# Performance work log

Measured on AMD Instinct MI355X. Metric: run time of the kernel, lower is better.

Reference implementation:

```python
import jax, jax.numpy as jnp
import numpy as np

EPS = 1e-5

def _bn(t, gamma, beta):
    # training-mode BatchNorm2d: stats over (B,H,W), biased variance
    mean = jnp.mean(t, axis=(0, 2, 3), keepdims=True)
    var = jnp.var(t, axis=(0, 2, 3), keepdims=True)
    tn = (t - mean) * jax.lax.rsqrt(var + EPS)
    return tn * gamma[None, :, None, None] + beta[None, :, None, None]

def setup_inputs() -> dict:
    key = jax.random.key(0)
    ks = jax.random.split(key, 8)
    B, C, H, W = 16, 256, 64, 64
    u, k, v = 4, 16, 256
    s = 1.0 / np.sqrt(C)
    x = jax.random.normal(ks[0], (B, C, H, W), dtype=jnp.float32)
    Wq = jax.random.normal(ks[1], (k, C), dtype=jnp.float32) * s
    bq = jax.random.normal(ks[2], (k,), dtype=jnp.float32) * 0.01
    Wk = jax.random.normal(ks[3], (u * k, C), dtype=jnp.float32) * s
    bk = jax.random.normal(ks[4], (u * k,), dtype=jnp.float32) * 0.01
    Wv = jax.random.normal(ks[5], (u * v, C), dtype=jnp.float32) * s
    bv = jax.random.normal(ks[6], (u * v,), dtype=jnp.float32) * 0.01
    gamma_q = jnp.ones((k,), dtype=jnp.float32)
    beta_q = jnp.zeros((k,), dtype=jnp.float32)
    gamma_v = jnp.ones((u * v,), dtype=jnp.float32)
    beta_v = jnp.zeros((u * v,), dtype=jnp.float32)
    return {"x": x, "Wq": Wq, "bq": bq, "Wk": Wk, "bk": bk, "Wv": Wv, "bv": bv,
            "gamma_q": gamma_q, "beta_q": beta_q, "gamma_v": gamma_v, "beta_v": beta_v}

def reference(x, Wq, bq, Wk, bk, Wv, bv, gamma_q, beta_q, gamma_v, beta_v):
    B, C, H, W = x.shape
    k = Wq.shape[0]
    u = 4
    v = Wv.shape[0] // u
    # 1x1 convs as channel contractions
    Q = jnp.einsum('oc,bchw->bohw', Wq, x) + bq[None, :, None, None]   # [B,k,H,W]
    K = jnp.einsum('oc,bchw->bohw', Wk, x) + bk[None, :, None, None]   # [B,u*k,H,W]
    V = jnp.einsum('oc,bchw->bohw', Wv, x) + bv[None, :, None, None]   # [B,u*v,H,W]
    Q = _bn(Q, gamma_q, beta_q)
    V = _bn(V, gamma_v, beta_v)
    m = H * W
    Q = Q.reshape(B, k, m)          # [B,k,m]
    K = K.reshape(B, u, k, m)       # [B,u,k,m]
    V = V.reshape(B, u, v, m)       # [B,u,v,m]
    K = jax.nn.softmax(K, axis=3)
    context = jnp.einsum('bukm,buvm->bkv', K, V)   # [B,k,v]
    y = jnp.einsum('bkn,bkv->bvn', Q, context)     # [B,v,m]
    return y.reshape(B, v, H, W)
```

## Files before the change

kernel.cpp:

```cpp
#include <hip/hip_runtime.h>
#include <hip/hip_bf16.h>

typedef short s16x8 __attribute__((ext_vector_type(8)));
typedef short s16x4 __attribute__((ext_vector_type(4)));
typedef float f32x4 __attribute__((ext_vector_type(4)));
typedef unsigned u32;
typedef u32 u32x2 __attribute__((ext_vector_type(2)));

#define DI __device__ __forceinline__

constexpr int BB = 16;
constexpr int CC = 256;
constexpr int MM = 4096;
constexpr int KD = 16;
constexpr int UK = 64;
constexpr float EPSV = 1e-5f;

DI unsigned short f2bf(float f) {
  union { float f; unsigned u; } v; v.f = f;
  unsigned r = v.u + 0x7FFFu + ((v.u >> 16) & 1u);
  return (unsigned short)(r >> 16);
}
DI float bflo(u32 v) { union { u32 u; float f; } w; w.u = v << 16; return w.f; }
DI float bfhi(u32 v) { union { u32 u; float f; } w; w.u = v & 0xFFFF0000u; return w.f; }

__global__ __launch_bounds__(256) void k_cvt(const float* __restrict__ x,
    unsigned short* __restrict__ xbf, float* __restrict__ xsump) {
  int bid = blockIdx.x;
  size_t base = (size_t)bid * MM;
  int t = threadIdx.x;
  float s = 0.f;
#pragma unroll
  for (int i = 0; i < 4; ++i) {
    size_t idx = base + (size_t)(i * 256 + t) * 4;
    float4 v = *(const float4*)(x + idx);
    s16x4 c;
    c[0] = (short)f2bf(v.x); c[1] = (short)f2bf(v.y);
    c[2] = (short)f2bf(v.z); c[3] = (short)f2bf(v.w);
    *(s16x4*)&xbf[idx] = c;
    s += v.x + v.y + v.z + v.w;
  }
#pragma unroll
  for (int o = 32; o; o >>= 1) s += __shfl_down(s, o);
  __shared__ float red[4];
  if ((t & 63) == 0) red[t >> 6] = s;
  __syncthreads();
  if (t == 0) xsump[bid] = red[0] + red[1] + red[2] + red[3];
}

__global__ __launch_bounds__(512) void k_gxx(const unsigned short* __restrict__ xbf,
                                             u32* __restrict__ part) {
  int b = blockIdx.x >> 4, mc = blockIdx.x & 15;
  int m0 = mc * 256;
  __shared__ short lds[2][256 * 72];
  int t = threadIdx.x, w = t >> 6, l = t & 63;
  int wr = w >> 2, wc = w & 3;
  int lrow = l & 15, lk8 = (l >> 4) * 8;
  int srow = t >> 3, sseg = (t & 7) * 8;

  const unsigned short* gsrc = xbf + ((size_t)(b * CC + srow)) * MM + m0 + sseg;

  s16x8 rg[4];
#pragma unroll
  for (int i = 0; i < 4; ++i)
    rg[i] = *(const s16x8*)(gsrc + (size_t)i * 64 * MM);
#pragma unroll
  for (int i = 0; i < 4; ++i)
    *(s16x8*)&lds[0][(srow + i * 64) * 72 + sseg] = rg[i];

  f32x4 acc[8][4];
#pragma unroll
  for (int i = 0; i < 8; ++i)
#pragma unroll
    for (int j = 0; j < 4; ++j) acc[i][j] = (f32x4)0.f;

#pragma unroll
  for (int ks = 0; ks < 4; ++ks) {
    __syncthreads();
    if (ks < 3) {
#pragma unroll
      for (int i = 0; i < 4; ++i)
        rg[i] = *(const s16x8*)(gsrc + (size_t)i * 64 * MM + (ks + 1) * 64);
    }
    int buf = ks & 1;
#pragma unroll
    for (int half = 0; half < 2; ++half) {
      s16x8 af[8], bf[4];
#pragma unroll
      for (int i = 0; i < 8; ++i)
        af[i] = *(const s16x8*)&lds[buf][(wr * 128 + i * 16 + lrow) * 72 + half * 32 + lk8];
#pragma unroll
      for (int j = 0; j < 4; ++j)
        bf[j] = *(const s16x8*)&lds[buf][(wc * 64 + j * 16 + lrow) * 72 + half * 32 + lk8];
#pragma unroll
      for (int i = 0; i < 8; ++i)
#pragma unroll
        for (int j = 0; j < 4; ++j)
          acc[i][j] = __builtin_amdgcn_mfma_f32_16x16x32_bf16(af[i], bf[j], acc[i][j], 0, 0, 0);
    }
    if (ks < 3) {
#pragma unroll
      for (int i = 0; i < 4; ++i)
        *(s16x8*)&lds[buf ^ 1][(srow + i * 64) * 72 + sseg] = rg[i];
    }
  }

  size_t pb = (size_t)blockIdx.x * 32768;
#pragma unroll
  for (int i = 0; i < 8; ++i)
#pragma unroll
    for (int j = 0; j < 4; ++j) {
      int tau = (w * 8 + i) * 4 + j;
      u32x2 pk;
      pk[0] = (u32)f2bf(acc[i][j][0]) | ((u32)f2bf(acc[i][j][1]) << 16);
      pk[1] = (u32)f2bf(acc[i][j][2]) | ((u32)f2bf(acc[i][j][3]) << 16);
      *(u32x2*)&part[pb + tau * 128 + l * 2] = pk;
    }
}

__global__ __launch_bounds__(256) void k_gred(const u32* __restrict__ part,
                                              float* __restrict__ G) {
  int q = blockIdx.x * 256 + threadIdx.x;
  float s0 = 0.f, s1 = 0.f;
#pragma unroll 8
  for (int p = 0; p < 256; ++p) {
    u32 v = part[(size_t)p * 32768 + q];
    s0 += bflo(v);
    s1 += bfhi(v);
  }
  int r2 = q & 1, l = (q >> 1) & 63, tau = q >> 7;
  int j = tau & 3, i = (tau >> 2) & 7, w = tau >> 5;
  int wr = w >> 2, wc = w & 3;
  int row = wr * 128 + i * 16 + (l >> 4) * 4 + r2 * 2;
  int col = wc * 64 + j * 16 + (l & 15);
  G[row * 256 + col] = s0;
  G[(row + 1) * 256 + col] = s1;
}

__global__ __launch_bounds__(256) void k_proj(const unsigned short* __restrict__ xbf,
    const float* __restrict__ Wq, const float* __restrict__ bq,
    const float* __restrict__ Wk, const float* __restrict__ bk,
    float* __restrict__ Kb, float* __restrict__ Qb) {
  int b = blockIdx.x >> 5, mc = blockIdx.x & 31;
  int gm0 = mc * 128;
  __shared__ short wlds[80 * 264];
  __shared__ u32 xt[128 * 17];
  int t = threadIdx.x;
  int w = t >> 6, l = t & 63;
  int lrow = l & 15, lk = l >> 4;

#pragma unroll 4
  for (int o = 0; o < 80; ++o) {
    float v = (o < 64) ? Wk[o * CC + t] : Wq[(o - 64) * CC + t];
    wlds[o * 264 + t] = (short)f2bf(v);
  }

  f32x4 acc[5][2];
#pragma unroll
  for (int i = 0; i < 5; ++i) { acc[i][0] = (f32x4)0.f; acc[i][1] = (f32x4)0.f; }

  int c2 = t >> 4;
  int mq = t & 15;

  for (int ks = 0; ks < 8; ++ks) {
    int c0 = ks * 32;
    __syncthreads();
#pragma unroll
    for (int mb = 0; mb < 128; mb += 64) {
      int m = mb + mq * 4;
      const unsigned short* p0 = xbf + ((size_t)(b * CC + c0 + 2 * c2)) * MM + gm0 + m;
      s16x4 v0 = *(const s16x4*)p0;
      s16x4 v1 = *(const s16x4*)(p0 + MM);
      xt[(m + 0) * 17 + c2] = (u32)(unsigned short)v0[0] | ((u32)(unsigned short)v1[0] << 16);
      xt[(m + 1) * 17 + c2] = (u32)(unsigned short)v0[1] | ((u32)(unsigned short)v1[1] << 16);
      xt[(m + 2) * 17 + c2] = (u32)(unsigned short)v0[2] | ((u32)(unsigned short)v1[2] << 16);
      xt[(m + 3) * 17 + c2] = (u32)(unsigned short)v0[3] | ((u32)(unsigned short)v1[3] << 16);
    }
    __syncthreads();
    union { s16x8 v; u32 wd[4]; } bfr[2];
#pragma unroll
    for (int j = 0; j < 2; ++j) {
      int ml = w * 32 + j * 16 + lrow;
#pragma unroll
      for (int i = 0; i < 4; ++i) bfr[j].wd[i] = xt[ml * 17 + lk * 4 + i];
    }
#pragma unroll
    for (int ot = 0; ot < 5; ++ot) {
      s16x8 af = *(const s16x8*)&wlds[(ot * 16 + lrow) * 264 + c0 + lk * 8];
      acc[ot][0] = __builtin_amdgcn_mfma_f32_16x16x32_bf16(af, bfr[0].v, acc[ot][0], 0, 0, 0);
      acc[ot][1] = __builtin_amdgcn_mfma_f32_16x16x32_bf16(af, bfr[1].v, acc[ot][1], 0, 0, 0);
    }
  }

#pragma unroll
  for (int ot = 0; ot < 5; ++ot)
#pragma unroll
    for (int j = 0; j < 2; ++j)
#pragma unroll
      for (int r = 0; r < 4; ++r) {
        int o = ot * 16 + lk * 4 + r;
        int m = gm0 + w * 32 + j * 16 + lrow;
        float val = acc[ot][j][r];
        if (o < 64) Kb[((size_t)(b * UK + o)) * MM + m] = val + bk[o];
        else        Qb[((size_t)(b * KD + o - 64)) * MM + m] = val + bq[o - 64];
      }
}

__global__ __launch_bounds__(256) void k_sstats(const float* __restrict__ Kb,
    float* __restrict__ rmax, float* __restrict__ rsum) {
  int r = blockIdx.x;
  int t = threadIdx.x;
  const float4* p = (const float4*)(Kb + (size_t)r * MM);
  float4 v[4];
  float mx = -3.4e38f;
#pragma unroll
  for (int i = 0; i < 4; ++i) {
    v[i] = p[i * 256 + t];
    mx = fmaxf(mx, fmaxf(fmaxf(v[i].x, v[i].y), fmaxf(v[i].z, v[i].w)));
  }
#pragma unroll
  for (int o = 32; o; o >>= 1) mx = fmaxf(mx, __shfl_xor(mx, o));
  __shared__ float red[4];
  int w = t >> 6;
  if ((t & 63) == 0) red[w] = mx;
  __syncthreads();
  mx = fmaxf(fmaxf(red[0], red[1]), fmaxf(red[2], red[3]));
  float s = 0.f;
#pragma unroll
  for (int i = 0; i < 4; ++i)
    s += __expf(v[i].x - mx) + __expf(v[i].y - mx) +
         __expf(v[i].z - mx) + __expf(v[i].w - mx);
#pragma unroll
  for (int o = 32; o; o >>= 1) s += __shfl_xor(s, o);
  __syncthreads();
  if ((t & 63) == 0) red[w] = s;
  __syncthreads();
  if (t == 0) {
    rmax[r] = mx;
    rsum[r] = red[0] + red[1] + red[2] + red[3];
  }
}

__global__ __launch_bounds__(256) void k_fin(const float* __restrict__ G,
    const float* __restrict__ xsump,
    const float* __restrict__ Wv, const float* __restrict__ bv,
    const float* __restrict__ gv, const float* __restrict__ btv,
    const float* __restrict__ Wq, const float* __restrict__ bq,
    const float* __restrict__ gq, const float* __restrict__ btq,
    float* __restrict__ AV, float* __restrict__ BVa,
    float* __restrict__ AQ, float* __restrict__ BQa) {
  int t = threadIdx.x, w = t >> 6, l = t & 63;
  int o0 = blockIdx.x * 4;
  __shared__ float lw[4][256];
#pragma unroll
  for (int oo = 0; oo < 4; ++oo) {
    int o = o0 + oo;
    lw[oo][t] = (o < 1024) ? Wv[(size_t)o * CC + t] : Wq[(size_t)(o - 1024) * CC + t];
  }
  __syncthreads();

  float4 w4[4];
#pragma unroll
  for (int oo = 0; oo < 4; ++oo) w4[oo] = *(const float4*)&lw[oo][4 * l];

  float qf[4] = {0.f, 0.f, 0.f, 0.f};
#pragma unroll 4
  for (int i = 0; i < 64; ++i) {
    int r = i * 4 + w;
    float4 g4 = *(const float4*)(G + (size_t)r * CC + 4 * l);
#pragma unroll
    for (int oo = 0; oo < 4; ++oo) {
      float d = g4.x * w4[oo].x + g4.y * w4[oo].y + g4.z * w4[oo].z + g4.w * w4[oo].w;
      qf[oo] = fmaf(lw[oo][r], d, qf[oo]);
    }
  }

  float xs = 0.f;
#pragma unroll
  for (int bb = 0; bb < 16; ++bb) xs += xsump[bb * 256 + t];
  float sx[4];
#pragma unroll
  for (int oo = 0; oo < 4; ++oo) sx[oo] = lw[oo][t] * xs;

#pragma unroll
  for (int oo = 0; oo < 4; ++oo)
#pragma unroll
    for (int od = 32; od; od >>= 1) {
      qf[oo] += __shfl_xor(qf[oo], od);
      sx[oo] += __shfl_xor(sx[oo], od);
    }
  __shared__ float rq[4][4], rs[4][4];
  if (l == 0)
#pragma unroll
    for (int oo = 0; oo < 4; ++oo) { rq[w][oo] = qf[oo]; rs[w][oo] = sx[oo]; }
  __syncthreads();
  if (t < 4) {
    int oo = t, o = o0 + oo;
    float q = rq[0][oo] + rq[1][oo] + rq[2][oo] + rq[3][oo];
    float s = rs[0][oo] + rs[1][oo] + rs[2][oo] + rs[3][oo];
    float bias, gamma, beta; float *pa, *pb;
    if (o < 1024) { bias = bv[o]; gamma = gv[o]; beta = btv[o]; pa = AV + o; pb = BVa + o; }
    else { int oi = o - 1024; bias = bq[oi]; gamma = gq[oi]; beta = btq[oi]; pa = AQ + oi; pb = BQa + oi; }
    const float invN = 1.f / 65536.f;
    float mean = s * invN + bias;
    float e2 = q * invN + 2.f * bias * s * invN + bias * bias;
    float var = e2 - mean * mean;
    float a = gamma * rsqrtf(var + EPSV);
    *pa = a;
    *pb = beta - mean * a;
  }
}

__global__ __launch_bounds__(256) void k_xp(const unsigned short* __restrict__ xbf,
    const float* __restrict__ Kb, const float* __restrict__ rmax,
    float* __restrict__ xpp) {
  int b = blockIdx.x >> 4, kc = blockIdx.x & 15;
  int kbase = kc * 256;
  __shared__ short la[64][40];
  __shared__ short lb[256][40];
  int t = threadIdx.x, w = t >> 6, l = t & 63;
  int lrow = l & 15, lk = (l >> 4) * 8;

  f32x4 acc[4][4];
#pragma unroll
  for (int i = 0; i < 4; ++i)
#pragma unroll
    for (int j = 0; j < 4; ++j) acc[i][j] = (f32x4)0.f;

  for (int ks = 0; ks < 8; ++ks) {
    int k0 = kbase + ks * 32;
    __syncthreads();
    {
      int r = t >> 2, sg = (t & 3) * 8;
      const float4* src = (const float4*)(Kb + ((size_t)(b * UK + r)) * MM + k0 + sg);
      float rm = rmax[b * UK + r];
      s16x8 wv;
#pragma unroll
      for (int i = 0; i < 2; ++i) {
        float4 v = src[i];
        wv[i * 4 + 0] = (short)f2bf(__expf(v.x - rm));
        wv[i * 4 + 1] = (short)f2bf(__expf(v.y - rm));
        wv[i * 4 + 2] = (short)f2bf(__expf(v.z - rm));
        wv[i * 4 + 3] = (short)f2bf(__expf(v.w - rm));
      }
      *(s16x8*)&la[r][sg] = wv;
    }
#pragma unroll
    for (int i = 0; i < 4; ++i) {
      int r = i * 64 + (t >> 2), sg = (t & 3) * 8;
      s16x8 v = *(const s16x8*)&xbf[((size_t)(b * CC + r)) * MM + k0 + sg];
      *(s16x8*)&lb[r][sg] = v;
    }
    __syncthreads();
    s16x8 af[4], bfr[4];
#pragma unroll
    for (int i = 0; i < 4; ++i) af[i] = *(const s16x8*)&la[i * 16 + lrow][lk];
#pragma unroll
    for (int j = 0; j < 4; ++j) bfr[j] = *(const s16x8*)&lb[w * 64 + j * 16 + lrow][lk];
#pragma unroll
    for (int i = 0; i < 4; ++i)
#pragma unroll
      for (int j = 0; j < 4; ++j)
        acc[i][j] = __builtin_amdgcn_mfma_f32_16x16x32_bf16(af[i], bfr[j], acc[i][j], 0, 0, 0);
  }
  float* dst = xpp + (size_t)blockIdx.x * UK * CC;
#pragma unroll
  for (int i = 0; i < 4; ++i)
#pragma unroll
    for (int j = 0; j < 4; ++j)
#pragma unroll
      for (int r = 0; r < 4; ++r) {
        int row = i * 16 + (l >> 4) * 4 + r;
        int col = w * 64 + j * 16 + lrow;
        dst[row * 256 + col] = acc[i][j][r];
      }
}

__global__ __launch_bounds__(256) void k_xpn(const float* __restrict__ xpp,
    const float* __restrict__ rsum, unsigned short* __restrict__ xpn) {
  int b = blockIdx.x >> 4, kk = blockIdx.x & 15;
  int t = threadIdx.x;
  unsigned short* dst = xpn + ((size_t)(b * 16 + kk)) * 1024;
#pragma unroll
  for (int u = 0; u < 4; ++u) {
    int row = u * 16 + kk;
    float s = 0.f;
#pragma unroll
    for (int kc = 0; kc < 16; ++kc)
      s += xpp[((size_t)(b * 16 + kc) * UK + row) * CC + t];
    s /= rsum[b * UK + row];
    dst[u * 256 + t] = f2bf(s);
  }
}

__global__ __launch_bounds__(256) void k_wvs(const float* __restrict__ Wv,
    const float* __restrict__ AV, unsigned short* __restrict__ wvs) {
  int ch = blockIdx.x;
  int t = threadIdx.x;
  float a = AV[ch];
  wvs[(size_t)ch * CC + t] = f2bf(a * Wv[(size_t)ch * CC + t]);
}

__global__ __launch_bounds__(64) void k_ctx2(const unsigned short* __restrict__ xpn,
    const unsigned short* __restrict__ wvs,
    const float* __restrict__ AV, const float* __restrict__ bv,
    const float* __restrict__ BVa, float* __restrict__ CTX) {
  int mt = blockIdx.x >> 3, nt = blockIdx.x & 7;
  int m0 = mt * 32, n0 = nt * 32;
  int l = threadIdx.x;
  int lrow = l & 15, lk8 = (l >> 4) * 8;

  f32x4 acc[2][2];
#pragma unroll
  for (int i = 0; i < 2; ++i)
#pragma unroll
    for (int j = 0; j < 2; ++j) acc[i][j] = (f32x4)0.f;

#pragma unroll 4
  for (int k0 = 0; k0 < 1024; k0 += 32) {
    int u = k0 >> 8, c0 = k0 & 255;
    s16x8 a0 = *(const s16x8*)&xpn[(size_t)(m0 + lrow) * 1024 + k0 + lk8];
    s16x8 a1 = *(const s16x8*)&xpn[(size_t)(m0 + 16 + lrow) * 1024 + k0 + lk8];
    s16x8 b0 = *(const s16x8*)&wvs[(size_t)(u * 256 + n0 + lrow) * CC + c0 + lk8];
    s16x8 b1 = *(const s16x8*)&wvs[(size_t)(u * 256 + n0 + 16 + lrow) * CC + c0 + lk8];
    acc[0][0] = __builtin_amdgcn_mfma_f32_16x16x32_bf16(a0, b0, acc[0][0], 0, 0, 0);
    acc[0][1] = __builtin_amdgcn_mfma_f32_16x16x32_bf16(a0, b1, acc[0][1], 0, 0, 0);
    acc[1][0] = __builtin_amdgcn_mfma_f32_16x16x32_bf16(a1, b0, acc[1][0], 0, 0, 0);
    acc[1][1] = __builtin_amdgcn_mfma_f32_16x16x32_bf16(a1, b1, acc[1][1], 0, 0, 0);
  }

  float cst[2];
#pragma unroll
  for (int j = 0; j < 2; ++j) {
    int vv = n0 + j * 16 + lrow;
    float s = 0.f;
#pragma unroll
    for (int u = 0; u < 4; ++u) {
      int ch = u * 256 + vv;
      s += AV[ch] * bv[ch] + BVa[ch];
    }
    cst[j] = s;
  }

#pragma unroll
  for (int i = 0; i < 2; ++i)
#pragma unroll
    for (int j = 0; j < 2; ++j)
#pragma unroll
      for (int r = 0; r < 4; ++r) {
        int row = m0 + i * 16 + (l >> 4) * 4 + r;
        int col = n0 + j * 16 + lrow;
        CTX[(size_t)row * 256 + col] = acc[i][j][r] + cst[j];
      }
}

__global__ __launch_bounds__(256) void k_y(const float* __restrict__ Qb,
    const float* __restrict__ CTX,
    const float* __restrict__ AQ, const float* __restrict__ BQa,
    float* __restrict__ y) {
  int b = blockIdx.x >> 4, nc = blockIdx.x & 15;
  int m = nc * 256 + threadIdx.x;
  float qn[16];
#pragma unroll
  for (int kk = 0; kk < 16; ++kk)
    qn[kk] = AQ[kk] * Qb[((size_t)b * KD + kk) * MM + m] + BQa[kk];
  const float* cb = CTX + (size_t)b * KD * 256;
  float* yo = y + (size_t)b * 256 * MM + m;
#pragma unroll 4
  for (int vv = 0; vv < 256; ++vv) {
    float acc = 0.f;
#pragma unroll
    for (int kk = 0; kk < 16; ++kk)
      acc = fmaf(qn[kk], cb[kk * 256 + vv], acc);
    yo[(size_t)vv * MM] = acc;
  }
}

extern "C" void kernel_launch(void* const* d_in, const int* in_sizes, int n_in,
                              void* d_out, int out_size, void* d_ws, size_t ws_size,
                              hipStream_t stream) {
  const float* x   = (const float*)d_in[0];
  const float* Wq  = (const float*)d_in[1];
  const float* bq  = (const float*)d_in[2];
  const float* Wk  = (const float*)d_in[3];
  const float* bk  = (const float*)d_in[4];
  const float* Wv  = (const float*)d_in[5];
  const float* bv  = (const float*)d_in[6];
  const float* gq  = (const float*)d_in[7];
  const float* btq = (const float*)d_in[8];
  const float* gv  = (const float*)d_in[9];
  const float* btv = (const float*)d_in[10];
  float* out = (float*)d_out;
  float* ws  = (float*)d_ws;

  float* G     = ws;
  float* XSUMP = ws + 65536;
  float* RMAX  = ws + 69632;
  float* RSUM  = ws + 70656;
  float* AV    = ws + 71680;
  float* BVa   = ws + 72704;
  float* AQ    = ws + 73728;
  float* BQa   = ws + 73744;
  float* CTX   = ws + 73984;
  float* XPP   = ws + 139520;
  float* KB    = ws + 4333824;
  float* QB    = ws + 8528128;
  u32*  PART   = (u32*)(ws + 139520);
  unsigned short* XBF = (unsigned short*)(ws + 9576704);
  unsigned short* XPN = (unsigned short*)(ws + 17965312);
  unsigned short* WVS = (unsigned short*)(ws + 18096384);

  k_cvt   <<<4096, 256, 0, stream>>>(x, XBF, XSUMP);
  k_gxx   <<<256,  512, 0, stream>>>(XBF, PART);
  k_gred  <<<128,  256, 0, stream>>>(PART, G);
  k_proj  <<<512,  256, 0, stream>>>(XBF, Wq, bq, Wk, bk, KB, QB);
  k_sstats<<<1024, 256, 0, stream>>>(KB, RMAX, RSUM);
  k_fin   <<<260,  256, 0, stream>>>(G, XSUMP, Wv, bv, gv, btv, Wq, bq, gq, btq,
                                     AV, BVa, AQ, BQa);
  k_xp    <<<256,  256, 0, stream>>>(XBF, KB, RMAX, XPP);
  k_xpn   <<<256,  256, 0, stream>>>(XPP, RSUM, XPN);
  k_wvs   <<<1024, 256, 0, stream>>>(Wv, AV, WVS);
  k_ctx2  <<<64,   64,  0, stream>>>(XPN, WVS, AV, bv, BVa, CTX);
  k_y     <<<256,  256, 0, stream>>>(QB, CTX, AQ, BQa, out);
}
```

Baseline: 145.5 us.

## Fuse bf16 conversion into Gram kernel, fold softmax stats into projection, store K/Q as bf16

The fp32-to-bf16 conversion of x and the per-channel sums move into the Gram-matrix kernel, so x is read once instead of being converted in a separate pass. The projection kernel now writes K and Q as bf16 and computes per-tile online softmax max/sum, which a small merge kernel combines. This replaces the full-row statistics pass over fp32 K. The xpn and wvs kernels are merged into one launch. Fewer launches and less global traffic are the aim, at the cost of storing K and Q at bf16 precision and a larger xsump reduction in k_fin.

```diff
diff --git a/kernel.cpp b/kernel.cpp
--- a/kernel.cpp
+++ b/kernel.cpp
@@ -21,35 +21,23 @@
   unsigned r = v.u + 0x7FFFu + ((v.u >> 16) & 1u);
   return (unsigned short)(r >> 16);
 }
+DI float bfu(unsigned short u) { union { u32 u; float f; } w; w.u = (u32)u << 16; return w.f; }
 DI float bflo(u32 v) { union { u32 u; float f; } w; w.u = v << 16; return w.f; }
 DI float bfhi(u32 v) { union { u32 u; float f; } w; w.u = v & 0xFFFF0000u; return w.f; }
 
-__global__ __launch_bounds__(256) void k_cvt(const float* __restrict__ x,
-    unsigned short* __restrict__ xbf, float* __restrict__ xsump) {
-  int bid = blockIdx.x;
-  size_t base = (size_t)bid * MM;
-  int t = threadIdx.x;
-  float s = 0.f;
-#pragma unroll
-  for (int i = 0; i < 4; ++i) {
-    size_t idx = base + (size_t)(i * 256 + t) * 4;
-    float4 v = *(const float4*)(x + idx);
-    s16x4 c;
-    c[0] = (short)f2bf(v.x); c[1] = (short)f2bf(v.y);
-    c[2] = (short)f2bf(v.z); c[3] = (short)f2bf(v.w);
-    *(s16x4*)&xbf[idx] = c;
-    s += v.x + v.y + v.z + v.w;
-  }
-#pragma unroll
-  for (int o = 32; o; o >>= 1) s += __shfl_down(s, o);
-  __shared__ float red[4];
-  if ((t & 63) == 0) red[t >> 6] = s;
-  __syncthreads();
-  if (t == 0) xsump[bid] = red[0] + red[1] + red[2] + red[3];
-}
-
-__global__ __launch_bounds__(512) void k_gxx(const unsigned short* __restrict__ xbf,
-                                             u32* __restrict__ part) {
+DI s16x8 cvt8(const float4 a, const float4 b, float& s) {
+  s16x8 c;
+  c[0] = (short)f2bf(a.x); c[1] = (short)f2bf(a.y);
+  c[2] = (short)f2bf(a.z); c[3] = (short)f2bf(a.w);
+  c[4] = (short)f2bf(b.x); c[5] = (short)f2bf(b.y);
+  c[6] = (short)f2bf(b.z); c[7] = (short)f2bf(b.w);
+  s += a.x + a.y + a.z + a.w + b.x + b.y + b.z + b.w;
+  return c;
+}
+
+__global__ __launch_bounds__(512) void k_gcv(const float* __restrict__ x,
+    unsigned short* __restrict__ xbf, float* __restrict__ xsump,
+    u32* __restrict__ part) {
   int b = blockIdx.x >> 4, mc = blockIdx.x & 15;
   int m0 = mc * 256;
   __shared__ short lds[2][256 * 72];
@@ -58,15 +46,24 @@
   int lrow = l & 15, lk8 = (l >> 4) * 8;
   int srow = t >> 3, sseg = (t & 7) * 8;
 
-  const unsigned short* gsrc = xbf + ((size_t)(b * CC + srow)) * MM + m0 + sseg;
-
-  s16x8 rg[4];
-#pragma unroll
-  for (int i = 0; i < 4; ++i)
-    rg[i] = *(const s16x8*)(gsrc + (size_t)i * 64 * MM);
-#pragma unroll
-  for (int i = 0; i < 4; ++i)
-    *(s16x8*)&lds[0][(srow + i * 64) * 72 + sseg] = rg[i];
+  const float* gsrc = x + ((size_t)(b * CC + srow)) * MM + m0 + sseg;
+  unsigned short* xdst = xbf + ((size_t)(b * CC + srow)) * MM + m0 + sseg;
+
+  float rs4[4] = {0.f, 0.f, 0.f, 0.f};
+  float4 rf[4][2];
+
+#pragma unroll
+  for (int i = 0; i < 4; ++i) {
+    const float* p = gsrc + (size_t)i * 64 * MM;
+    rf[i][0] = *(const float4*)p;
+    rf[i][1] = *(const float4*)(p + 4);
+  }
+#pragma unroll
+  for (int i = 0; i < 4; ++i) {
+    s16x8 c = cvt8(rf[i][0], rf[i][1], rs4[i]);
+    *(s16x8*)&lds[0][(srow + i * 64) * 72 + sseg] = c;
+    *(s16x8*)&xdst[(size_t)i * 64 * MM] = c;
+  }
 
   f32x4 acc[8][4];
 #pragma unroll
@@ -79,8 +76,11 @@
     __syncthreads();
     if (ks < 3) {
 #pragma unroll
-      for (int i = 0; i < 4; ++i)
-        rg[i] = *(const s16x8*)(gsrc + (size_t)i * 64 * MM + (ks + 1) * 64);
+      for (int i = 0; i < 4; ++i) {
+        const float* p = gsrc + (size_t)i * 64 * MM + (ks + 1) * 64;
+        rf[i][0] = *(const float4*)p;
+        rf[i][1] = *(const float4*)(p + 4);
+      }
     }
     int buf = ks & 1;
 #pragma unroll
@@ -100,9 +100,19 @@
     }
     if (ks < 3) {
 #pragma unroll
-      for (int i = 0; i < 4; ++i)
-        *(s16x8*)&lds[buf ^ 1][(srow + i * 64) * 72 + sseg] = rg[i];
-    }
+      for (int i = 0; i < 4; ++i) {
+        s16x8 c = cvt8(rf[i][0], rf[i][1], rs4[i]);
+        *(s16x8*)&lds[buf ^ 1][(srow + i * 64) * 72 + sseg] = c;
+        *(s16x8*)&xdst[(size_t)i * 64 * MM + (ks + 1) * 64] = c;
+      }
+    }
+  }
+
+#pragma unroll
+  for (int i = 0; i < 4; ++i) {
+    float s = rs4[i];
+    s += __shfl_xor(s, 1); s += __shfl_xor(s, 2); s += __shfl_xor(s, 4);
+    if ((t & 7) == 0) xsump[blockIdx.x * 256 + srow + i * 64] = s;
   }
 
   size_t pb = (size_t)blockIdx.x * 32768;
@@ -140,11 +150,13 @@
 __global__ __launch_bounds__(256) void k_proj(const unsigned short* __restrict__ xbf,
     const float* __restrict__ Wq, const float* __restrict__ bq,
     const float* __restrict__ Wk, const float* __restrict__ bk,
-    float* __restrict__ Kb, float* __restrict__ Qb) {
+    unsigned short* __restrict__ Kbf, unsigned short* __restrict__ Qbf,
+    float* __restrict__ pstat) {
   int b = blockIdx.x >> 5, mc = blockIdx.x & 31;
   int gm0 = mc * 128;
   __shared__ short wlds[80 * 264];
   __shared__ u32 xt[128 * 17];
+  __shared__ float smax[4][64], ssum[4][64];
   int t = threadIdx.x;
   int w = t >> 6, l = t & 63;
   int lrow = l & 15, lk = l >> 4;
@@ -192,53 +204,66 @@
     }
   }
 
-#pragma unroll
-  for (int ot = 0; ot < 5; ++ot)
-#pragma unroll
-    for (int j = 0; j < 2; ++j)
-#pragma unroll
-      for (int r = 0; r < 4; ++r) {
-        int o = ot * 16 + lk * 4 + r;
-        int m = gm0 + w * 32 + j * 16 + lrow;
-        float val = acc[ot][j][r];
-        if (o < 64) Kb[((size_t)(b * UK + o)) * MM + m] = val + bk[o];
-        else        Qb[((size_t)(b * KD + o - 64)) * MM + m] = val + bq[o - 64];
-      }
-}
-
-__global__ __launch_bounds__(256) void k_sstats(const float* __restrict__ Kb,
+  int mcol = gm0 + w * 32 + lrow;
+#pragma unroll
+  for (int ot = 0; ot < 4; ++ot)
+#pragma unroll
+    for (int r = 0; r < 4; ++r) {
+      int o = ot * 16 + lk * 4 + r;
+      float bias = bk[o];
+      unsigned short u0 = f2bf(acc[ot][0][r] + bias);
+      unsigned short u1 = f2bf(acc[ot][1][r] + bias);
+      size_t rowoff = ((size_t)(b * UK + o)) * MM;
+      Kbf[rowoff + mcol] = u0;
+      Kbf[rowoff + mcol + 16] = u1;
+      float rv0 = bfu(u0), rv1 = bfu(u1);
+      float mx = fmaxf(rv0, rv1);
+      mx = fmaxf(mx, __shfl_xor(mx, 1));
+      mx = fmaxf(mx, __shfl_xor(mx, 2));
+      mx = fmaxf(mx, __shfl_xor(mx, 4));
+      mx = fmaxf(mx, __shfl_xor(mx, 8));
+      float se = __expf(rv0 - mx) + __expf(rv1 - mx);
+      se += __shfl_xor(se, 1);
+      se += __shfl_xor(se, 2);
+      se += __shfl_xor(se, 4);
+      se += __shfl_xor(se, 8);
+      if (lrow == 0) { smax[w][o] = mx; ssum[w][o] = se; }
+    }
+#pragma unroll
+  for (int r = 0; r < 4; ++r) {
+    int oq = lk * 4 + r;
+    float bias = bq[oq];
+    size_t rowoff = ((size_t)(b * KD + oq)) * MM;
+    Qbf[rowoff + mcol] = f2bf(acc[4][0][r] + bias);
+    Qbf[rowoff + mcol + 16] = f2bf(acc[4][1][r] + bias);
+  }
+  __syncthreads();
+  if (t < 64) {
+    float m0_ = smax[0][t], m1_ = smax[1][t], m2_ = smax[2][t], m3_ = smax[3][t];
+    float mm = fmaxf(fmaxf(m0_, m1_), fmaxf(m2_, m3_));
+    float ss = ssum[0][t] * __expf(m0_ - mm) + ssum[1][t] * __expf(m1_ - mm) +
+               ssum[2][t] * __expf(m2_ - mm) + ssum[3][t] * __expf(m3_ - mm);
+    size_t po = ((size_t)blockIdx.x * 64 + t) * 2;
+    pstat[po] = mm;
+    pstat[po + 1] = ss;
+  }
+}
+
+__global__ __launch_bounds__(64) void k_pmerge(const float* __restrict__ pstat,
     float* __restrict__ rmax, float* __restrict__ rsum) {
-  int r = blockIdx.x;
-  int t = threadIdx.x;
-  const float4* p = (const float4*)(Kb + (size_t)r * MM);
-  float4 v[4];
-  float mx = -3.4e38f;
-#pragma unroll
-  for (int i = 0; i < 4; ++i) {
-    v[i] = p[i * 256 + t];
-    mx = fmaxf(mx, fmaxf(fmaxf(v[i].x, v[i].y), fmaxf(v[i].z, v[i].w)));
-  }
-#pragma unroll
-  for (int o = 32; o; o >>= 1) mx = fmaxf(mx, __shfl_xor(mx, o));
-  __shared__ float red[4];
-  int w = t >> 6;
-  if ((t & 63) == 0) red[w] = mx;
-  __syncthreads();
-  mx = fmaxf(fmaxf(red[0], red[1]), fmaxf(red[2], red[3]));
-  float s = 0.f;
-#pragma unroll
-  for (int i = 0; i < 4; ++i)
-    s += __expf(v[i].x - mx) + __expf(v[i].y - mx) +
-         __expf(v[i].z - mx) + __expf(v[i].w - mx);
-#pragma unroll
-  for (int o = 32; o; o >>= 1) s += __shfl_xor(s, o);
-  __syncthreads();
-  if ((t & 63) == 0) red[w] = s;
-  __syncthreads();
-  if (t == 0) {
-    rmax[r] = mx;
-    rsum[r] = red[0] + red[1] + red[2] + red[3];
-  }
+  int b = blockIdx.x, o = threadIdx.x;
+  float mm = -3.4e38f;
+#pragma unroll 8
+  for (int mc = 0; mc < 32; ++mc)
+    mm = fmaxf(mm, pstat[((size_t)((b * 32 + mc) * 64 + o)) * 2]);
+  float ss = 0.f;
+#pragma unroll 8
+  for (int mc = 0; mc < 32; ++mc) {
+    size_t po = ((size_t)((b * 32 + mc) * 64 + o)) * 2;
+    ss += pstat[po + 1] * __expf(pstat[po] - mm);
+  }
+  rmax[b * 64 + o] = mm;
+  rsum[b * 64 + o] = ss;
 }
 
 __global__ __launch_bounds__(256) void k_fin(const float* __restrict__ G,
@@ -276,8 +301,8 @@
   }
 
   float xs = 0.f;
-#pragma unroll
-  for (int bb = 0; bb < 16; ++bb) xs += xsump[bb * 256 + t];
+#pragma unroll 8
+  for (int p = 0; p < 256; ++p) xs += xsump[p * 256 + t];
   float sx[4];
 #pragma unroll
   for (int oo = 0; oo < 4; ++oo) sx[oo] = lw[oo][t] * xs;
@@ -312,7 +337,7 @@
 }
 
 __global__ __launch_bounds__(256) void k_xp(const unsigned short* __restrict__ xbf,
-    const float* __restrict__ Kb, const float* __restrict__ rmax,
+    const unsigned short* __restrict__ Kbf, const float* __restrict__ rmax,
     float* __restrict__ xpp) {
   int b = blockIdx.x >> 4, kc = blockIdx.x & 15;
   int kbase = kc * 256;
@@ -332,17 +357,12 @@
     __syncthreads();
     {
       int r = t >> 2, sg = (t & 3) * 8;
-      const float4* src = (const float4*)(Kb + ((size_t)(b * UK + r)) * MM + k0 + sg);
+      s16x8 kv = *(const s16x8*)&Kbf[((size_t)(b * UK + r)) * MM + k0 + sg];
       float rm = rmax[b * UK + r];
       s16x8 wv;
 #pragma unroll
-      for (int i = 0; i < 2; ++i) {
-        float4 v = src[i];
-        wv[i * 4 + 0] = (short)f2bf(__expf(v.x - rm));
-        wv[i * 4 + 1] = (short)f2bf(__expf(v.y - rm));
-        wv[i * 4 + 2] = (short)f2bf(__expf(v.z - rm));
-        wv[i * 4 + 3] = (short)f2bf(__expf(v.w - rm));
-      }
+      for (int i = 0; i < 8; ++i)
+        wv[i] = (short)f2bf(__expf(bfu((unsigned short)kv[i]) - rm));
       *(s16x8*)&la[r][sg] = wv;
     }
 #pragma unroll
@@ -376,29 +396,29 @@
       }
 }
 
-__global__ __launch_bounds__(256) void k_xpn(const float* __restrict__ xpp,
-    const float* __restrict__ rsum, unsigned short* __restrict__ xpn) {
-  int b = blockIdx.x >> 4, kk = blockIdx.x & 15;
+__global__ __launch_bounds__(256) void k_prep(const float* __restrict__ xpp,
+    const float* __restrict__ rsum, const float* __restrict__ Wv,
+    const float* __restrict__ AV, unsigned short* __restrict__ xpn,
+    unsigned short* __restrict__ wvs) {
   int t = threadIdx.x;
-  unsigned short* dst = xpn + ((size_t)(b * 16 + kk)) * 1024;
-#pragma unroll
-  for (int u = 0; u < 4; ++u) {
-    int row = u * 16 + kk;
-    float s = 0.f;
-#pragma unroll
-    for (int kc = 0; kc < 16; ++kc)
-      s += xpp[((size_t)(b * 16 + kc) * UK + row) * CC + t];
-    s /= rsum[b * UK + row];
-    dst[u * 256 + t] = f2bf(s);
-  }
-}
-
-__global__ __launch_bounds__(256) void k_wvs(const float* __restrict__ Wv,
-    const float* __restrict__ AV, unsigned short* __restrict__ wvs) {
-  int ch = blockIdx.x;
-  int t = threadIdx.x;
-  float a = AV[ch];
-  wvs[(size_t)ch * CC + t] = f2bf(a * Wv[(size_t)ch * CC + t]);
+  if (blockIdx.x < 256) {
+    int b = blockIdx.x >> 4, kk = blockIdx.x & 15;
+    unsigned short* dst = xpn + ((size_t)(b * 16 + kk)) * 1024;
+#pragma unroll
+    for (int u = 0; u < 4; ++u) {
+      int row = u * 16 + kk;
+      float s = 0.f;
+#pragma unroll
+      for (int kc = 0; kc < 16; ++kc)
+        s += xpp[((size_t)(b * 16 + kc) * UK + row) * CC + t];
+      s /= rsum[b * UK + row];
+      dst[u * 256 + t] = f2bf(s);
+    }
+  } else {
+    int ch = blockIdx.x - 256;
+    float a = AV[ch];
+    wvs[(size_t)ch * CC + t] = f2bf(a * Wv[(size_t)ch * CC + t]);
+  }
 }
 
 __global__ __launch_bounds__(64) void k_ctx2(const unsigned short* __restrict__ xpn,
@@ -454,7 +474,7 @@
       }
 }
 
-__global__ __launch_bounds__(256) void k_y(const float* __restrict__ Qb,
+__global__ __launch_bounds__(256) void k_y(const unsigned short* __restrict__ Qbf,
     const float* __restrict__ CTX,
     const float* __restrict__ AQ, const float* __restrict__ BQa,
     float* __restrict__ y) {
@@ -463,7 +483,7 @@
   float qn[16];
 #pragma unroll
   for (int kk = 0; kk < 16; ++kk)
-    qn[kk] = AQ[kk] * Qb[((size_t)b * KD + kk) * MM + m] + BQa[kk];
+    qn[kk] = AQ[kk] * bfu(Qbf[((size_t)b * KD + kk) * MM + m]) + BQa[kk];
   const float* cb = CTX + (size_t)b * KD * 256;
   float* yo = y + (size_t)b * 256 * MM + m;
 #pragma unroll 4
@@ -495,31 +515,30 @@
 
   float* G     = ws;
   float* XSUMP = ws + 65536;
-  float* RMAX  = ws + 69632;
-  float* RSUM  = ws + 70656;
-  float* AV    = ws + 71680;
-  float* BVa   = ws + 72704;
-  float* AQ    = ws + 73728;
-  float* BQa   = ws + 73744;
-  float* CTX   = ws + 73984;
-  float* XPP   = ws + 139520;
-  float* KB    = ws + 4333824;
-  float* QB    = ws + 8528128;
-  u32*  PART   = (u32*)(ws + 139520);
-  unsigned short* XBF = (unsigned short*)(ws + 9576704);
-  unsigned short* XPN = (unsigned short*)(ws + 17965312);
-  unsigned short* WVS = (unsigned short*)(ws + 18096384);
-
-  k_cvt   <<<4096, 256, 0, stream>>>(x, XBF, XSUMP);
-  k_gxx   <<<256,  512, 0, stream>>>(XBF, PART);
+  float* PSTAT = ws + 131072;
+  float* RMAX  = ws + 196608;
+  float* RSUM  = ws + 197632;
+  float* AV    = ws + 198656;
+  float* BVa   = ws + 199680;
+  float* AQ    = ws + 200704;
+  float* BQa   = ws + 200720;
+  float* CTX   = ws + 200960;
+  u32*  PART   = (u32*)(ws + 266496);
+  float* XPP   = ws + 266496;
+  unsigned short* KBf = (unsigned short*)(ws + 4460800);
+  unsigned short* QBf = (unsigned short*)(ws + 6557952);
+  unsigned short* XBF = (unsigned short*)(ws + 8655104);
+  unsigned short* XPN = (unsigned short*)(ws + 17043712);
+  unsigned short* WVS = (unsigned short*)(ws + 17174784);
+
+  k_gcv   <<<256,  512, 0, stream>>>(x, XBF, XSUMP, PART);
   k_gred  <<<128,  256, 0, stream>>>(PART, G);
-  k_proj  <<<512,  256, 0, stream>>>(XBF, Wq, bq, Wk, bk, KB, QB);
-  k_sstats<<<1024, 256, 0, stream>>>(KB, RMAX, RSUM);
+  k_proj  <<<512,  256, 0, stream>>>(XBF, Wq, bq, Wk, bk, KBf, QBf, PSTAT);
+  k_pmerge<<<16,   64,  0, stream>>>(PSTAT, RMAX, RSUM);
   k_fin   <<<260,  256, 0, stream>>>(G, XSUMP, Wv, bv, gv, btv, Wq, bq, gq, btq,
                                      AV, BVa, AQ, BQa);
-  k_xp    <<<256,  256, 0, stream>>>(XBF, KB, RMAX, XPP);
-  k_xpn   <<<256,  256, 0, stream>>>(XPP, RSUM, XPN);
-  k_wvs   <<<1024, 256, 0, stream>>>(Wv, AV, WVS);
+  k_xp    <<<256,  256, 0, stream>>>(XBF, KBf, RMAX, XPP);
+  k_prep  <<<1280, 256, 0, stream>>>(XPP, RSUM, Wv, AV, XPN, WVS);
   k_ctx2  <<<64,   64,  0, stream>>>(XPN, WVS, AV, bv, BVa, CTX);
-  k_y     <<<256,  256, 0, stream>>>(QB, CTX, AQ, BQa, out);
-}
+  k_y     <<<256,  256, 0, stream>>>(QBf, CTX, AQ, BQa, out);
+}
```

Measured after the change: 163.0 us. 1.12x slower.
